# Kernel tuning notes

Hardware: AMD Instinct MI355X
Metric: run time of the kernel (lower is better)

## Reference

```python
import jax, jax.numpy as jnp
import numpy as np

BATCH = 32768
TEXT_DIM = 384
HIDDEN = 256
NUM_LAYERS = 4
NUM_VERTS = 12
K_NN = 6


def _build_template():
    """Icosphere vertices (12, normalized) and row-normalized kNN adjacency (12,12)."""
    phi = (1.0 + 5.0 ** 0.5) / 2.0
    v = np.array([
        [-1, phi, 0], [1, phi, 0], [-1, -phi, 0], [1, -phi, 0],
        [0, -1, phi], [0, 1, phi], [0, -1, -phi], [0, 1, -phi],
        [phi, 0, -1], [phi, 0, 1], [-phi, 0, -1], [-phi, 0, 1],
    ], dtype=np.float32)
    v = v / np.linalg.norm(v, axis=1, keepdims=True)
    dist = np.linalg.norm(v[:, None, :] - v[None, :, :], axis=-1)  # (12,12)
    # k+1 smallest per row; index 0 is self (distance 0), skip it
    idx = np.argsort(dist, axis=1, kind='stable')[:, 1:K_NN + 1]
    adj = np.zeros((NUM_VERTS, NUM_VERTS), dtype=np.float32)
    rows = np.repeat(np.arange(NUM_VERTS), K_NN)
    adj[rows, idx.reshape(-1)] = 1.0
    adj = adj / (adj.sum(axis=1, keepdims=True) + 1e-6)
    return jnp.asarray(v), jnp.asarray(adj)


def setup_inputs() -> dict:
    key = jax.random.key(0)
    ks = jax.random.split(key, 8)
    template, adjacency = _build_template()
    scale = 0.02
    return {
        "text_emb": jax.random.normal(ks[0], (BATCH, TEXT_DIM), dtype=jnp.float32),
        "W_text": jax.random.normal(ks[1], (TEXT_DIM, HIDDEN), dtype=jnp.float32) * scale,
        "b_text": jnp.zeros((HIDDEN,), dtype=jnp.float32),
        "W_gnn": jax.random.normal(ks[2], (NUM_LAYERS, HIDDEN, HIDDEN), dtype=jnp.float32) * scale,
        "b_gnn": jnp.zeros((NUM_LAYERS, HIDDEN), dtype=jnp.float32),
        "W_out": jax.random.normal(ks[3], (HIDDEN, 3), dtype=jnp.float32) * scale,
        "b_out": jnp.zeros((3,), dtype=jnp.float32),
        "adjacency": adjacency,   # (12,12) buffer
        "template": template,     # (12,3) buffer
    }


def reference(text_emb, W_text, b_text, W_gnn, b_gnn, W_out, b_out, adjacency, template):
    # text projection -> broadcast to all nodes
    tf = text_emb @ W_text + b_text                       # (B, H)
    B = text_emb.shape[0]
    h = jnp.broadcast_to(tf[:, None, :], (B, NUM_VERTS, HIDDEN))
    # GNN layers: aggregate (shared adjacency across batch), project, relu
    for l in range(NUM_LAYERS):
        agg = jnp.einsum('nm,bmd->bnd', adjacency, h)     # (B, 12, H)
        h = jax.nn.relu(agg @ W_gnn[l] + b_gnn[l])
    displacements = h @ W_out + b_out                     # (B, 12, 3)
    return template[None, :, :] + displacements
```

## Files before the change

### kernel.cpp

```cpp
#include <hip/hip_runtime.h>
#include <stdint.h>

#define TD      384
#define HID     256
#define NLAYERS 4

typedef __bf16 bf16;
typedef __attribute__((ext_vector_type(8))) __bf16 bf16x8;
typedef __attribute__((ext_vector_type(4))) float f32x4;

union FragU { uint4 u; bf16x8 f; };

__device__ inline f32x4 mfma16(bf16x8 a, bf16x8 b, f32x4 c) {
  return __builtin_amdgcn_mfma_f32_16x16x32_bf16(a, b, c, 0, 0, 0);
}

__global__ __launch_bounds__(256) void prep_kernel(
    const float* __restrict__ W_text, const float* __restrict__ W_gnn,
    const float* __restrict__ W_out,
    bf16* __restrict__ wt_text, bf16* __restrict__ wt_gnn, float* __restrict__ wot)
{
  __shared__ float tile[32][33];
  int bid = blockIdx.x;
  int tx = threadIdx.x & 31, ty = threadIdx.x >> 5;
  const float* in; bf16* out; int R, C, tR, tC;
  if (bid < 96) {
    in = W_text; out = wt_text; R = TD; C = HID;
    tC = bid & 7; tR = bid >> 3;
  } else if (bid < 352) {
    int b = bid - 96; int l = b >> 6; int t = b & 63;
    in = W_gnn + l*HID*HID; out = wt_gnn + l*HID*HID; R = HID; C = HID;
    tC = t & 7; tR = t >> 3;
  } else {
    for (int t = threadIdx.x; t < 3*HID; t += 256) {
      int comp = t >> 8, k = t & 255;
      wot[comp*HID + k] = W_out[k*3 + comp];
    }
    return;
  }
  #pragma unroll
  for (int i = 0; i < 4; i++)
    tile[ty + i*8][tx] = in[(tR*32 + ty + i*8)*C + tC*32 + tx];
  __syncthreads();
  #pragma unroll
  for (int i = 0; i < 4; i++)
    out[(tC*32 + ty + i*8)*R + tR*32 + tx] = (bf16)tile[tx][ty + i*8];
}

__global__ __launch_bounds__(256, 2) void mesh_kernel(
    const float* __restrict__ text,
    const bf16* __restrict__ wt_text,
    const bf16* __restrict__ wt_gnn,
    const float* __restrict__ b_text,
    const float* __restrict__ b_gnn,
    const float* __restrict__ wot,
    const float* __restrict__ b_out,
    const float* __restrict__ tmpl,
    float* __restrict__ out)
{
  __shared__ __align__(16) unsigned char smem[49152];
  unsigned char* wchunk = smem + 32768;

  const int tid  = threadIdx.x;
  const int lane = tid & 63;
  const int w    = tid >> 6;
  const int cc   = lane & 15;
  const int qq   = lane >> 4;
  const int mh   = w >> 1;
  const int nh   = w & 1;
  const int rowbase = blockIdx.x * 64;

  f32x4 acc[2][8];

  auto stage = [&](const bf16* wsrc, int rowbytes, int ks) {
    const char* gbase = (const char*)wsrc + ks*64;
    #pragma unroll
    for (int i = 0; i < 4; i++) {
      int sbase = w*256 + i*64;
      int s = sbase + lane;
      int n = s >> 2;
      int q = (s - (n >> 2)) & 3;
      const char* g = gbase + n*rowbytes + q*16;
      __builtin_amdgcn_global_load_lds(
          (__attribute__((address_space(1))) void*)(g),
          (__attribute__((address_space(3))) void*)(wchunk + sbase*16),
          16, 0, 0);
    }
  };

  auto read_b = [&](int nt) -> bf16x8 {
    int n = nh*128 + nt*16 + cc;
    int s = n*4 + ((qq + (n >> 2)) & 3);
    FragU fu; fu.u = *(const uint4*)(wchunk + s*16);
    return fu.f;
  };

  auto read_a = [&](int mt, int ks) -> bf16x8 {
    int m = mh*32 + mt*16 + cc;
    int po = (ks*4 + qq) ^ (m & 7);
    FragU fu; fu.u = *(const uint4*)(smem + m*512 + po*16);
    return fu.f;
  };

  auto zero_acc = [&]() {
    f32x4 z = {0.f, 0.f, 0.f, 0.f};
    #pragma unroll
    for (int mt = 0; mt < 2; mt++)
      #pragma unroll
      for (int nt = 0; nt < 8; nt++)
        acc[mt][nt] = z;
  };

  auto write_h = [&](const float* bias_ptr, bool relu) {
    float bias[8];
    #pragma unroll
    for (int nt = 0; nt < 8; nt++) bias[nt] = bias_ptr[nh*128 + nt*16 + cc];
    #pragma unroll
    for (int mt = 0; mt < 2; mt++) {
      #pragma unroll
      for (int nt = 0; nt < 8; nt++) {
        int col = nh*128 + nt*16 + cc;
        #pragma unroll
        for (int r = 0; r < 4; r++) {
          int m = mh*32 + mt*16 + qq*4 + r;
          float v = acc[mt][nt][r] + bias[nt];
          if (relu) v = fmaxf(v, 0.f);
          int po = (col >> 3) ^ (m & 7);
          *(bf16*)(smem + m*512 + po*16 + (col & 7)*2) = (bf16)v;
        }
      }
    }
  };

  zero_acc();
  stage(wt_text, TD*2, 0);
  for (int ks = 0; ks < TD/32; ks++) {
    __syncthreads();
    bf16x8 a0, a1;
    #pragma unroll
    for (int mt = 0; mt < 2; mt++) {
      int row = rowbase + mh*32 + mt*16 + cc;
      const float4* p = (const float4*)(text + row*TD + ks*32 + qq*8);
      float4 x = p[0], y = p[1];
      bf16x8 f;
      f[0]=(bf16)x.x; f[1]=(bf16)x.y; f[2]=(bf16)x.z; f[3]=(bf16)x.w;
      f[4]=(bf16)y.x; f[5]=(bf16)y.y; f[6]=(bf16)y.z; f[7]=(bf16)y.w;
      if (mt == 0) a0 = f; else a1 = f;
    }
    #pragma unroll
    for (int nt = 0; nt < 8; nt++) {
      bf16x8 b = read_b(nt);
      acc[0][nt] = mfma16(a0, b, acc[0][nt]);
      acc[1][nt] = mfma16(a1, b, acc[1][nt]);
    }
    __syncthreads();
    if (ks + 1 < TD/32) stage(wt_text, TD*2, ks + 1);
  }
  write_h(b_text, false);

  for (int l = 0; l < NLAYERS; l++) {
    const bf16* wsrc = wt_gnn + l*HID*HID;
    zero_acc();
    stage(wsrc, HID*2, 0);
    for (int ks = 0; ks < HID/32; ks++) {
      __syncthreads();
      bf16x8 a0 = read_a(0, ks);
      bf16x8 a1 = read_a(1, ks);
      #pragma unroll
      for (int nt = 0; nt < 8; nt++) {
        bf16x8 b = read_b(nt);
        acc[0][nt] = mfma16(a0, b, acc[0][nt]);
        acc[1][nt] = mfma16(a1, b, acc[1][nt]);
      }
      __syncthreads();
      if (ks + 1 < HID/32) stage(wsrc, HID*2, ks + 1);
    }
    write_h(b_gnn + l*HID, true);
  }

  float* dispBuf = (float*)(wchunk);
  __syncthreads();
  if (tid < 192) {
    int comp = tid >> 6;
    int r = tid & 63;
    const float4* wrow = (const float4*)(wot + comp*HID);
    float s = 0.f;
    #pragma unroll 4
    for (int o = 0; o < 32; o++) {
      int po = o ^ (r & 7);
      FragU fu; fu.u = *(const uint4*)(smem + r*512 + po*16);
      float4 w0 = wrow[2*o], w1 = wrow[2*o + 1];
      s += (float)fu.f[0]*w0.x + (float)fu.f[1]*w0.y + (float)fu.f[2]*w0.z + (float)fu.f[3]*w0.w;
      s += (float)fu.f[4]*w1.x + (float)fu.f[5]*w1.y + (float)fu.f[6]*w1.z + (float)fu.f[7]*w1.w;
    }
    dispBuf[r*3 + comp] = s + b_out[comp];
  }
  __syncthreads();
  #pragma unroll
  for (int ii = 0; ii < 9; ii++) {
    int i = ii*256 + tid;
    int row = i / 36;
    int j = i - row*36;
    out[rowbase*36 + i] = tmpl[j] + dispBuf[row*3 + j % 3];
  }
}

extern "C" void kernel_launch(void* const* d_in, const int* in_sizes, int n_in,
                              void* d_out, int out_size, void* d_ws, size_t ws_size,
                              hipStream_t stream) {
  const float* text   = (const float*)d_in[0];
  const float* W_text = (const float*)d_in[1];
  const float* b_text = (const float*)d_in[2];
  const float* W_gnn  = (const float*)d_in[3];
  const float* b_gnn  = (const float*)d_in[4];
  const float* W_out  = (const float*)d_in[5];
  const float* b_out  = (const float*)d_in[6];
  const float* tmpl   = (const float*)d_in[8];
  float* outp = (float*)d_out;

  bf16* wt_text = (bf16*)d_ws;
  bf16* wt_gnn  = wt_text + 256*384;
  float* wot    = (float*)(wt_gnn + 4*256*256);

  prep_kernel<<<353, 256, 0, stream>>>(W_text, W_gnn, W_out, wt_text, wt_gnn, wot);
  mesh_kernel<<<32768/64, 256, 0, stream>>>(text, wt_text, wt_gnn, b_text, b_gnn,
                                            wot, b_out, tmpl, outp);
}
```

Measured before the change: 143.1 us.

## Load weight fragments directly from global in MFMA order, double-buffer activations

The prep kernel now writes weights pre-packed in MFMA B-fragment order, so each lane reads its B operand with one 16-byte global load instead of staging through LDS with global_load_lds. The main loops register-prefetch the next k-step's A and B fragments and drop the two barriers per k-step. Activations ping-pong between two padded LDS buffers, with the row stride padded to 528 bytes in place of the XOR swizzle, leaving one barrier per layer. The cost is more global/L2 traffic for weights per wave and higher register pressure from the prefetch buffers.

```diff
diff --git a/kernel.cpp b/kernel.cpp
--- a/kernel.cpp
+++ b/kernel.cpp
@@ -4,12 +4,14 @@
 #define TD      384
 #define HID     256
 #define NLAYERS 4
+#define ROWB    528
 
 typedef __bf16 bf16;
 typedef __attribute__((ext_vector_type(8))) __bf16 bf16x8;
 typedef __attribute__((ext_vector_type(4))) float f32x4;
 
 union FragU { uint4 u; bf16x8 f; };
+union PackU { uint4 u; bf16 v[8]; };
 
 __device__ inline f32x4 mfma16(bf16x8 a, bf16x8 b, f32x4 c) {
   return __builtin_amdgcn_mfma_f32_16x16x32_bf16(a, b, c, 0, 0, 0);
@@ -20,31 +22,33 @@
     const float* __restrict__ W_out,
     bf16* __restrict__ wt_text, bf16* __restrict__ wt_gnn, float* __restrict__ wot)
 {
-  __shared__ float tile[32][33];
-  int bid = blockIdx.x;
-  int tx = threadIdx.x & 31, ty = threadIdx.x >> 5;
-  const float* in; bf16* out; int R, C, tR, tC;
-  if (bid < 96) {
-    in = W_text; out = wt_text; R = TD; C = HID;
-    tC = bid & 7; tR = bid >> 3;
-  } else if (bid < 352) {
-    int b = bid - 96; int l = b >> 6; int t = b & 63;
-    in = W_gnn + l*HID*HID; out = wt_gnn + l*HID*HID; R = HID; C = HID;
-    tC = t & 7; tR = t >> 3;
+  int bid = blockIdx.x, tid = threadIdx.x;
+  if (bid < 48) {
+    int idx = bid * 256 + tid;
+    int cc = idx & 15, c = idx >> 4;
+    int n16 = c / 48, oct = c - n16 * 48;
+    int n = n16 * 16 + cc;
+    PackU pk;
+    #pragma unroll
+    for (int j = 0; j < 8; j++) pk.v[j] = (bf16)W_text[(oct * 8 + j) * HID + n];
+    *(uint4*)(wt_text + idx * 8) = pk.u;
+  } else if (bid < 176) {
+    int idx = (bid - 48) * 256 + tid;
+    int cc = idx & 15, c = idx >> 4;
+    int l = c >> 9, c2 = c & 511;
+    int oct = c2 & 31;
+    int n = (c2 >> 5) * 16 + cc;
+    const float* base = W_gnn + l * HID * HID;
+    PackU pk;
+    #pragma unroll
+    for (int j = 0; j < 8; j++) pk.v[j] = (bf16)base[(oct * 8 + j) * HID + n];
+    *(uint4*)(wt_gnn + idx * 8) = pk.u;
   } else {
-    for (int t = threadIdx.x; t < 3*HID; t += 256) {
+    for (int t = tid; t < 3 * HID; t += 256) {
       int comp = t >> 8, k = t & 255;
-      wot[comp*HID + k] = W_out[k*3 + comp];
-    }
-    return;
-  }
-  #pragma unroll
-  for (int i = 0; i < 4; i++)
-    tile[ty + i*8][tx] = in[(tR*32 + ty + i*8)*C + tC*32 + tx];
-  __syncthreads();
-  #pragma unroll
-  for (int i = 0; i < 4; i++)
-    out[(tC*32 + ty + i*8)*R + tR*32 + tx] = (bf16)tile[tx][ty + i*8];
+      wot[comp * HID + k] = W_out[k * 3 + comp];
+    }
+  }
 }
 
 __global__ __launch_bounds__(256, 2) void mesh_kernel(
@@ -58,8 +62,9 @@
     const float* __restrict__ tmpl,
     float* __restrict__ out)
 {
-  __shared__ __align__(16) unsigned char smem[49152];
-  unsigned char* wchunk = smem + 32768;
+  __shared__ __align__(16) unsigned char smem[2 * 64 * ROWB];
+  unsigned char* hb0 = smem;
+  unsigned char* hb1 = smem + 64 * ROWB;
 
   const int tid  = threadIdx.x;
   const int lane = tid & 63;
@@ -69,139 +74,144 @@
   const int mh   = w >> 1;
   const int nh   = w & 1;
   const int rowbase = blockIdx.x * 64;
+  const int voff = qq * 256 + cc * 16;
 
   f32x4 acc[2][8];
-
-  auto stage = [&](const bf16* wsrc, int rowbytes, int ks) {
-    const char* gbase = (const char*)wsrc + ks*64;
-    #pragma unroll
-    for (int i = 0; i < 4; i++) {
-      int sbase = w*256 + i*64;
-      int s = sbase + lane;
-      int n = s >> 2;
-      int q = (s - (n >> 2)) & 3;
-      const char* g = gbase + n*rowbytes + q*16;
-      __builtin_amdgcn_global_load_lds(
-          (__attribute__((address_space(1))) void*)(g),
-          (__attribute__((address_space(3))) void*)(wchunk + sbase*16),
-          16, 0, 0);
-    }
-  };
-
-  auto read_b = [&](int nt) -> bf16x8 {
-    int n = nh*128 + nt*16 + cc;
-    int s = n*4 + ((qq + (n >> 2)) & 3);
-    FragU fu; fu.u = *(const uint4*)(wchunk + s*16);
-    return fu.f;
-  };
-
-  auto read_a = [&](int mt, int ks) -> bf16x8 {
-    int m = mh*32 + mt*16 + cc;
-    int po = (ks*4 + qq) ^ (m & 7);
-    FragU fu; fu.u = *(const uint4*)(smem + m*512 + po*16);
-    return fu.f;
-  };
 
   auto zero_acc = [&]() {
     f32x4 z = {0.f, 0.f, 0.f, 0.f};
     #pragma unroll
     for (int mt = 0; mt < 2; mt++)
       #pragma unroll
-      for (int nt = 0; nt < 8; nt++)
-        acc[mt][nt] = z;
-  };
-
-  auto write_h = [&](const float* bias_ptr, bool relu) {
-    float bias[8];
-    #pragma unroll
-    for (int nt = 0; nt < 8; nt++) bias[nt] = bias_ptr[nh*128 + nt*16 + cc];
+      for (int nt = 0; nt < 8; nt++) acc[mt][nt] = z;
+  };
+
+  auto loadB = [&](const char* wbase, int ks, bf16x8* B, int K8x256) {
+    #pragma unroll
+    for (int nt = 0; nt < 8; nt++) {
+      FragU fu; fu.u = *(const uint4*)(wbase + ks * 1024 + nt * K8x256);
+      B[nt] = fu.f;
+    }
+  };
+
+  auto loadA = [&](const unsigned char* src, int ks, bf16x8* A) {
     #pragma unroll
     for (int mt = 0; mt < 2; mt++) {
-      #pragma unroll
-      for (int nt = 0; nt < 8; nt++) {
-        int col = nh*128 + nt*16 + cc;
-        #pragma unroll
-        for (int r = 0; r < 4; r++) {
-          int m = mh*32 + mt*16 + qq*4 + r;
-          float v = acc[mt][nt][r] + bias[nt];
-          if (relu) v = fmaxf(v, 0.f);
-          int po = (col >> 3) ^ (m & 7);
-          *(bf16*)(smem + m*512 + po*16 + (col & 7)*2) = (bf16)v;
-        }
-      }
-    }
-  };
-
-  zero_acc();
-  stage(wt_text, TD*2, 0);
-  for (int ks = 0; ks < TD/32; ks++) {
-    __syncthreads();
-    bf16x8 a0, a1;
+      int m = mh * 32 + mt * 16 + cc;
+      FragU fu; fu.u = *(const uint4*)(src + m * ROWB + ks * 64 + qq * 16);
+      A[mt] = fu.f;
+    }
+  };
+
+  auto loadAtext = [&](int ks, bf16x8* A) {
     #pragma unroll
     for (int mt = 0; mt < 2; mt++) {
-      int row = rowbase + mh*32 + mt*16 + cc;
-      const float4* p = (const float4*)(text + row*TD + ks*32 + qq*8);
+      int row = rowbase + mh * 32 + mt * 16 + cc;
+      const float4* p = (const float4*)(text + row * TD + ks * 32 + qq * 8);
       float4 x = p[0], y = p[1];
       bf16x8 f;
       f[0]=(bf16)x.x; f[1]=(bf16)x.y; f[2]=(bf16)x.z; f[3]=(bf16)x.w;
       f[4]=(bf16)y.x; f[5]=(bf16)y.y; f[6]=(bf16)y.z; f[7]=(bf16)y.w;
-      if (mt == 0) a0 = f; else a1 = f;
-    }
-    #pragma unroll
-    for (int nt = 0; nt < 8; nt++) {
-      bf16x8 b = read_b(nt);
-      acc[0][nt] = mfma16(a0, b, acc[0][nt]);
-      acc[1][nt] = mfma16(a1, b, acc[1][nt]);
-    }
+      A[mt] = f;
+    }
+  };
+
+  auto write_h = [&](unsigned char* dst, const float* bias_ptr, bool relu) {
+    float bias[8];
+    #pragma unroll
+    for (int nt = 0; nt < 8; nt++) bias[nt] = bias_ptr[nh * 128 + nt * 16 + cc];
+    #pragma unroll
+    for (int mt = 0; mt < 2; mt++) {
+      #pragma unroll
+      for (int nt = 0; nt < 8; nt++) {
+        int col = nh * 128 + nt * 16 + cc;
+        #pragma unroll
+        for (int r = 0; r < 4; r++) {
+          int m = mh * 32 + mt * 16 + qq * 4 + r;
+          float v = acc[mt][nt][r] + bias[nt];
+          if (relu) v = fmaxf(v, 0.f);
+          *(bf16*)(dst + m * ROWB + col * 2) = (bf16)v;
+        }
+      }
+    }
+  };
+
+  {
+    const char* wbase = (const char*)wt_text + nh * 8 * 12288 + voff;
+    zero_acc();
+    bf16x8 A[2], B[8];
+    loadB(wbase, 0, B, 12288);
+    loadAtext(0, A);
+    #pragma unroll
+    for (int ks = 0; ks < TD / 32; ks++) {
+      bf16x8 An[2], Bn[8];
+      if (ks + 1 < TD / 32) { loadB(wbase, ks + 1, Bn, 12288); loadAtext(ks + 1, An); }
+      #pragma unroll
+      for (int nt = 0; nt < 8; nt++) {
+        acc[0][nt] = mfma16(A[0], B[nt], acc[0][nt]);
+        acc[1][nt] = mfma16(A[1], B[nt], acc[1][nt]);
+      }
+      if (ks + 1 < TD / 32) {
+        #pragma unroll
+        for (int nt = 0; nt < 8; nt++) B[nt] = Bn[nt];
+        A[0] = An[0]; A[1] = An[1];
+      }
+    }
+    write_h(hb0, b_text, false);
+  }
+  __syncthreads();
+
+  for (int l = 0; l < NLAYERS; l++) {
+    const unsigned char* src = (l & 1) ? hb1 : hb0;
+    unsigned char*       dst = (l & 1) ? hb0 : hb1;
+    const char* wbase = (const char*)(wt_gnn + l * HID * HID) + nh * 8 * 8192 + voff;
+    zero_acc();
+    bf16x8 A[2], B[8];
+    loadB(wbase, 0, B, 8192);
+    loadA(src, 0, A);
+    #pragma unroll
+    for (int ks = 0; ks < HID / 32; ks++) {
+      bf16x8 An[2], Bn[8];
+      if (ks + 1 < HID / 32) { loadB(wbase, ks + 1, Bn, 8192); loadA(src, ks + 1, An); }
+      #pragma unroll
+      for (int nt = 0; nt < 8; nt++) {
+        acc[0][nt] = mfma16(A[0], B[nt], acc[0][nt]);
+        acc[1][nt] = mfma16(A[1], B[nt], acc[1][nt]);
+      }
+      if (ks + 1 < HID / 32) {
+        #pragma unroll
+        for (int nt = 0; nt < 8; nt++) B[nt] = Bn[nt];
+        A[0] = An[0]; A[1] = An[1];
+      }
+    }
+    write_h(dst, b_gnn + l * HID, l < NLAYERS - 1 ? true : true);
     __syncthreads();
-    if (ks + 1 < TD/32) stage(wt_text, TD*2, ks + 1);
-  }
-  write_h(b_text, false);
-
-  for (int l = 0; l < NLAYERS; l++) {
-    const bf16* wsrc = wt_gnn + l*HID*HID;
-    zero_acc();
-    stage(wsrc, HID*2, 0);
-    for (int ks = 0; ks < HID/32; ks++) {
-      __syncthreads();
-      bf16x8 a0 = read_a(0, ks);
-      bf16x8 a1 = read_a(1, ks);
-      #pragma unroll
-      for (int nt = 0; nt < 8; nt++) {
-        bf16x8 b = read_b(nt);
-        acc[0][nt] = mfma16(a0, b, acc[0][nt]);
-        acc[1][nt] = mfma16(a1, b, acc[1][nt]);
-      }
-      __syncthreads();
-      if (ks + 1 < HID/32) stage(wsrc, HID*2, ks + 1);
-    }
-    write_h(b_gnn + l*HID, true);
-  }
-
-  float* dispBuf = (float*)(wchunk);
-  __syncthreads();
+  }
+
+  float* dispBuf = (float*)hb1;
+
   if (tid < 192) {
     int comp = tid >> 6;
     int r = tid & 63;
-    const float4* wrow = (const float4*)(wot + comp*HID);
+    const float4* wrow = (const float4*)(wot + comp * HID);
     float s = 0.f;
     #pragma unroll 4
     for (int o = 0; o < 32; o++) {
-      int po = o ^ (r & 7);
-      FragU fu; fu.u = *(const uint4*)(smem + r*512 + po*16);
-      float4 w0 = wrow[2*o], w1 = wrow[2*o + 1];
+      FragU fu; fu.u = *(const uint4*)(hb0 + r * ROWB + o * 16);
+      float4 w0 = wrow[2 * o], w1 = wrow[2 * o + 1];
       s += (float)fu.f[0]*w0.x + (float)fu.f[1]*w0.y + (float)fu.f[2]*w0.z + (float)fu.f[3]*w0.w;
       s += (float)fu.f[4]*w1.x + (float)fu.f[5]*w1.y + (float)fu.f[6]*w1.z + (float)fu.f[7]*w1.w;
     }
-    dispBuf[r*3 + comp] = s + b_out[comp];
+    dispBuf[r * 3 + comp] = s + b_out[comp];
   }
   __syncthreads();
+
   #pragma unroll
   for (int ii = 0; ii < 9; ii++) {
-    int i = ii*256 + tid;
+    int i = ii * 256 + tid;
     int row = i / 36;
-    int j = i - row*36;
-    out[rowbase*36 + i] = tmpl[j] + dispBuf[row*3 + j % 3];
+    int j = i - row * 36;
+    out[rowbase * 36 + i] = tmpl[j] + dispBuf[row * 3 + j % 3];
   }
 }
 
@@ -222,7 +232,7 @@
   bf16* wt_gnn  = wt_text + 256*384;
   float* wot    = (float*)(wt_gnn + 4*256*256);
 
-  prep_kernel<<<353, 256, 0, stream>>>(W_text, W_gnn, W_out, wt_text, wt_gnn, wot);
+  prep_kernel<<<177, 256, 0, stream>>>(W_text, W_gnn, W_out, wt_text, wt_gnn, wot);
   mesh_kernel<<<32768/64, 256, 0, stream>>>(text, wt_text, wt_gnn, b_text, b_gnn,
                                             wot, b_out, tmpl, outp);
 }
```

After: 139.0 us. 2.9% less time.
